# Kernel optimization log

Hardware: AMD Instinct MI355X
Metric: run time of the kernel (lower is better)

The kernel has to match this reference:

```python
import jax, jax.numpy as jnp
import numpy as np

EMBED = 8   # forced: combine_heads Linear(embed_dim, embed_dim) applied to 8-wire measurement
FFN = 32
B, S = 128, 8192
EPS = 1e-5


def _layernorm(x, g, b):
    m = x.mean(-1, keepdims=True)
    v = ((x - m) ** 2).mean(-1, keepdims=True)
    return (x - m) * jax.lax.rsqrt(v + EPS) * g + b


def setup_inputs() -> dict:
    key = jax.random.key(0)
    ks = jax.random.split(key, 8)

    def lin(k, fi, fo):
        return jax.random.normal(k, (fi, fo), jnp.float32) / np.sqrt(fi).astype(np.float32)

    return dict(
        x=jax.random.normal(ks[0], (B, S, EMBED), jnp.float32),
        Wq=lin(ks[1], EMBED, EMBED), bq=jnp.zeros((EMBED,), jnp.float32),
        theta_attn=jax.random.uniform(ks[2], (EMBED,), jnp.float32, -np.pi, np.pi),
        Wc=lin(ks[3], EMBED, EMBED), bc=jnp.zeros((EMBED,), jnp.float32),
        g1=jnp.ones((EMBED,), jnp.float32), beta1=jnp.zeros((EMBED,), jnp.float32),
        theta_ffn=jax.random.uniform(ks[4], (EMBED,), jnp.float32, -np.pi, np.pi),
        W1=lin(ks[5], EMBED, FFN), b1=jnp.zeros((FFN,), jnp.float32),
        W2=lin(ks[6], FFN, EMBED), b2=jnp.zeros((EMBED,), jnp.float32),
        g2=jnp.ones((EMBED,), jnp.float32), beta2=jnp.zeros((EMBED,), jnp.float32),
    )


def reference(x, Wq, bq, theta_attn, Wc, bc, g1, beta1,
              theta_ffn, W1, b1, W2, b2, g2, beta2):
    # --- MultiHeadAttentionQuantum (eval mode, dropout = identity) ---
    # q_linear; the 8-wire encoder consumes all 8 features of q per token.
    q = x @ Wq + bq                           # [B, S, 8]
    # Circuit per token: RX(q_i) then trainable RX(theta_i) on wire i -> RX(q_i+theta_i),
    # then CNOT ring (0->1,...,6->7, 7->0), then <Z_i>.
    # All-RX product state => basis probs p_i(1)=sin^2(a_i/2); CNOTs permute basis
    # states (prefix-XOR of bits), so analytically:
    #   <Z_k> = prod_{j=0..k} cos(a_j)  for k>=1;   <Z_0> = prod_{j=1..7} cos(a_j)
    ca = jnp.cos(q + theta_attn)              # [B, S, 8]
    z_rest = jnp.cumprod(ca, axis=-1)[..., 1:]
    z0 = jnp.prod(ca[..., 1:], axis=-1, keepdims=True)
    z = jnp.concatenate([z0, z_rest], axis=-1)
    attn_out = z @ Wc + bc                    # combine_heads

    x1 = _layernorm(x + attn_out, g1, beta1)

    # --- FeedForwardQuantum: RX(x_i) then RY(theta_i), no entanglers ->
    #     <Z_i> = cos(theta_i) * cos(x_i)  (product state, per-wire closed form)
    zf = jnp.cos(theta_ffn) * jnp.cos(x1)     # [B, S, 8]
    h = jax.nn.relu(zf @ W1 + b1)             # linear1 -> relu
    ffn_out = h @ W2 + b2                     # linear2

    return _layernorm(x1 + ffn_out, g2, beta2)
```

## Files before the change

kernel.cpp:

```cpp
#include <hip/hip_runtime.h>


#define NTOK   (128 * 8192)
#define NTHREADS 256
#define NBLOCKS  (NTOK / NTHREADS)
#define LN_EPS 1e-5f
#define INV2PI 0.15915494309189535f

typedef __fp16 half2_t __attribute__((ext_vector_type(2)));
typedef __fp16 half8_t __attribute__((ext_vector_type(8)));
typedef float  float4_t __attribute__((ext_vector_type(4)));

union PK  { unsigned u; half2_t h; };
union U4H { uint4 u; half8_t h; half2_t h2[4]; };

__device__ __forceinline__ float fast_cos_rev(float xrev) {
    return __builtin_amdgcn_cosf(xrev);
}
__device__ __forceinline__ float fast_cos(float x) {
    return __builtin_amdgcn_cosf(x * INV2PI);
}
__device__ __forceinline__ float fast_rsqrt(float x) {
    return __builtin_amdgcn_rsqf(x);
}
__device__ __forceinline__ unsigned packh2(float a, float b) {
    PK c; c.h = __builtin_amdgcn_cvt_pkrtz(a, b); return c.u;
}
__device__ __forceinline__ float dot2(half2_t a, unsigned bw, float c) {
    PK b; b.u = bw;
    return __builtin_amdgcn_fdot2(a, b.h, c, false);
}

__global__ void pack_weights(const float* __restrict__ Wq,
                             const float* __restrict__ W1,
                             const float* __restrict__ W2,
                             const float* __restrict__ Wc,
                             const float* __restrict__ bq,
                             const float* __restrict__ tha,
                             const float* __restrict__ thf,
                             unsigned* __restrict__ ws)
{
    int idx = threadIdx.x;
    if (idx < 32) {
        int k = idx >> 2, p = idx & 3;
        ws[idx] = packh2(Wq[(2 * p) * 8 + k] * INV2PI, Wq[(2 * p + 1) * 8 + k] * INV2PI);
    } else if (idx < 64) {
        int i2 = idx - 32;
        int kp = i2 >> 3, j = i2 & 7;
        ws[idx] = packh2(Wc[(2 * kp) * 8 + j], Wc[(2 * kp + 1) * 8 + j]);
    } else if (idx < 72) {
        int k = idx - 64;
        ws[idx] = __float_as_uint((bq[k] + tha[k]) * INV2PI);
    } else if (idx < 80) {
        int j = idx - 72;
        ws[idx] = __float_as_uint(__builtin_amdgcn_cosf(thf[j] * INV2PI));
    } else if (idx >= 128 && idx < 320) {
        int t  = (idx - 128) & 63;
        int tb = (idx - 128) >> 6;
        int n0 = t & 15, q = t >> 4;
        uint4 w = make_uint4(0u, 0u, 0u, 0u);
        unsigned r[4] = {0u, 0u, 0u, 0u};
        if (tb == 0) {
            if (q == 0)
                for (int p = 0; p < 4; ++p)
                    r[p] = packh2(W1[(2 * p) * 32 + n0], W1[(2 * p + 1) * 32 + n0]);
        } else if (tb == 1) {
            if (q == 0)
                for (int p = 0; p < 4; ++p)
                    r[p] = packh2(W1[(2 * p) * 32 + n0 + 16], W1[(2 * p + 1) * 32 + n0 + 16]);
        } else {
            if (n0 < 8)
                for (int p = 0; p < 4; ++p)
                    r[p] = packh2(W2[(8 * q + 2 * p) * 8 + n0], W2[(8 * q + 2 * p + 1) * 8 + n0]);
        }
        w.x = r[0]; w.y = r[1]; w.z = r[2]; w.w = r[3];
        reinterpret_cast<uint4*>(ws)[32 + tb * 64 + t] = w;
    }
}

__global__ __launch_bounds__(NTHREADS, 8)
void qtb_kernel(const float* __restrict__ x,
                const float* __restrict__ bc,
                const float* __restrict__ g1,  const float* __restrict__ be1,
                const float* __restrict__ b1,
                const float* __restrict__ b2,
                const float* __restrict__ g2,  const float* __restrict__ be2,
                const unsigned* __restrict__ wp,
                float* __restrict__ out)
{
    const int tid  = threadIdx.x;
    const int wave = tid >> 6;
    const int lane = tid & 63;
    const int col  = lane & 15;
    const int quad = lane >> 4;
    const int g    = blockIdx.x * NTHREADS + tid;

    const float4* px = reinterpret_cast<const float4*>(x) + (size_t)g * 2;
    float4 xa = px[0];
    float4 xb = px[1];

    const float* qb = reinterpret_cast<const float*>(wp + 64);
    const float* cf = reinterpret_cast<const float*>(wp + 72);

    __shared__ uint4    zbuf[4][64];
    __shared__ unsigned hbuf[4][16 * 20];
    __shared__ float    fbuf[4][64 * 9];

    const uint4* fr = reinterpret_cast<const uint4*>(wp);
    U4H B1a, B1b, B2;
    B1a.u = fr[32 + lane];
    B1b.u = fr[96 + lane];
    B2.u  = fr[160 + lane];
    const float b1a_s = b1[col];
    const float b1b_s = b1[col + 16];
    const float b2_s  = (col < 8) ? b2[col & 7] : 0.f;

    float xv[8];
    half2_t xp[4];
    xv[0] = xa.x; xv[1] = xa.y; xv[2] = xa.z; xv[3] = xa.w;
    xv[4] = xb.x; xv[5] = xb.y; xv[6] = xb.z; xv[7] = xb.w;
    xp[0] = __builtin_amdgcn_cvt_pkrtz(xa.x, xa.y);
    xp[1] = __builtin_amdgcn_cvt_pkrtz(xa.z, xa.w);
    xp[2] = __builtin_amdgcn_cvt_pkrtz(xb.x, xb.y);
    xp[3] = __builtin_amdgcn_cvt_pkrtz(xb.z, xb.w);

    float ca[8];
#pragma unroll
    for (int k = 0; k < 8; ++k) {
        float q = qb[k];
#pragma unroll
        for (int p = 0; p < 4; ++p) q = dot2(xp[p], wp[k * 4 + p], q);
        ca[k] = fast_cos_rev(q);
    }
    float attn[8];
#pragma unroll
    for (int j = 0; j < 8; ++j) attn[j] = bc[j];
    {
        float z[8];
        float cp  = ca[0];
        float cp1 = 1.0f;
#pragma unroll
        for (int k = 1; k < 8; ++k) {
            cp  *= ca[k];
            cp1 *= ca[k];
            z[k] = cp;
        }
        z[0] = cp1;
        half2_t zp[4];
#pragma unroll
        for (int p = 0; p < 4; ++p)
            zp[p] = __builtin_amdgcn_cvt_pkrtz(z[2 * p], z[2 * p + 1]);
#pragma unroll
        for (int p = 0; p < 4; ++p)
#pragma unroll
            for (int j = 0; j < 8; ++j)
                attn[j] = dot2(zp[p], wp[32 + p * 8 + j], attn[j]);
    }

    {
        float y[8];
        float s = 0.f;
#pragma unroll
        for (int j = 0; j < 8; ++j) { y[j] = xv[j] + attn[j]; s += y[j]; }
        float m = s * 0.125f;
        float v = 0.f;
#pragma unroll
        for (int j = 0; j < 8; ++j) { float d = y[j] - m; v += d * d; }
        float r = fast_rsqrt(v * 0.125f + LN_EPS);
        float zf[8];
#pragma unroll
        for (int j = 0; j < 8; ++j) {
            float x1 = (y[j] - m) * r * g1[j] + be1[j];
            xv[j] = x1;
            zf[j] = cf[j] * fast_cos(x1);
        }
        U4H zpk;
#pragma unroll
        for (int p = 0; p < 4; ++p)
            zpk.h2[p] = __builtin_amdgcn_cvt_pkrtz(zf[2 * p], zf[2 * p + 1]);
        zbuf[wave][lane] = zpk.u;
    }

    const unsigned psel = (quad < 2) ? 0x05040100u : 0x07060302u;
#pragma unroll
    for (int grp = 0; grp < 4; ++grp) {
        U4H A1; A1.u = zbuf[wave][grp * 16 + col];
        float4_t c1a = {b1a_s, b1a_s, b1a_s, b1a_s};
        float4_t c1b = {b1b_s, b1b_s, b1b_s, b1b_s};
        float4_t h0 = __builtin_amdgcn_mfma_f32_16x16x32_f16(A1.h, B1a.h, c1a, 0, 0, 0);
        float4_t h1 = __builtin_amdgcn_mfma_f32_16x16x32_f16(A1.h, B1b.h, c1b, 0, 0, 0);
#pragma unroll
        for (int r = 0; r < 4; ++r)
            hbuf[wave][(4 * quad + r) * 20 + col] =
                packh2(fmaxf(h0[r], 0.f), fmaxf(h1[r], 0.f));
        int hb = col * 20 + (quad & 1) * 8;
        uint4 w0 = *reinterpret_cast<const uint4*>(&hbuf[wave][hb]);
        uint4 w1 = *reinterpret_cast<const uint4*>(&hbuf[wave][hb + 4]);
        U4H A2;
        A2.u.x = __builtin_amdgcn_perm(w0.y, w0.x, psel);
        A2.u.y = __builtin_amdgcn_perm(w0.w, w0.z, psel);
        A2.u.z = __builtin_amdgcn_perm(w1.y, w1.x, psel);
        A2.u.w = __builtin_amdgcn_perm(w1.w, w1.z, psel);
        float4_t c2 = {b2_s, b2_s, b2_s, b2_s};
        float4_t f = __builtin_amdgcn_mfma_f32_16x16x32_f16(A2.h, B2.h, c2, 0, 0, 0);
        if (col < 8) {
#pragma unroll
            for (int r = 0; r < 4; ++r)
                fbuf[wave][(grp * 16 + 4 * quad + r) * 9 + col] = f[r];
        }
    }

    {
        float y[8];
        float s = 0.f;
#pragma unroll
        for (int j = 0; j < 8; ++j) {
            y[j] = xv[j] + fbuf[wave][lane * 9 + j];
            s += y[j];
        }
        float m = s * 0.125f;
        float v = 0.f;
#pragma unroll
        for (int j = 0; j < 8; ++j) { float d = y[j] - m; v += d * d; }
        float r = fast_rsqrt(v * 0.125f + LN_EPS);
        float o[8];
#pragma unroll
        for (int j = 0; j < 8; ++j) o[j] = (y[j] - m) * r * g2[j] + be2[j];
        float4* q = reinterpret_cast<float4*>(out) + (size_t)g * 2;
        q[0] = make_float4(o[0], o[1], o[2], o[3]);
        q[1] = make_float4(o[4], o[5], o[6], o[7]);
    }
}

extern "C" void kernel_launch(void* const* d_in, const int* in_sizes, int n_in,
                              void* d_out, int out_size, void* d_ws, size_t ws_size,
                              hipStream_t stream) {
    (void)in_sizes; (void)n_in; (void)ws_size; (void)out_size;
    unsigned* wp = (unsigned*)d_ws;
    pack_weights<<<1, 320, 0, stream>>>(
        (const float*)d_in[1],
        (const float*)d_in[9],
        (const float*)d_in[11],
        (const float*)d_in[4],
        (const float*)d_in[2],
        (const float*)d_in[3],
        (const float*)d_in[8],
        wp);
    qtb_kernel<<<NBLOCKS, NTHREADS, 0, stream>>>(
        (const float*)d_in[0],
        (const float*)d_in[5],
        (const float*)d_in[6],
        (const float*)d_in[7],
        (const float*)d_in[10],
        (const float*)d_in[12],
        (const float*)d_in[13],
        (const float*)d_in[14],
        wp,
        (float*)d_out);
}
```

Before: 115.0 us.

## Replace MFMA FFN with per-thread packed fp16 dot2 FFN

Drops the matrix-core path for the feed-forward layers, along with its LDS staging buffers and shuffles. Each thread now evaluates both FFN linears for its own token with packed fp16 dot2 instructions, reading the packed weights as uniform scalar loads from the workspace. This removes shared-memory traffic and cross-lane data movement. In exchange it raises per-thread VALU work (32x4 plus 8x16 dot2 ops) and register pressure.

```diff
diff --git a/kernel.cpp b/kernel.cpp
--- a/kernel.cpp
+++ b/kernel.cpp
@@ -8,11 +8,8 @@
 #define INV2PI 0.15915494309189535f
 
 typedef __fp16 half2_t __attribute__((ext_vector_type(2)));
-typedef __fp16 half8_t __attribute__((ext_vector_type(8)));
-typedef float  float4_t __attribute__((ext_vector_type(4)));
 
 union PK  { unsigned u; half2_t h; };
-union U4H { uint4 u; half8_t h; half2_t h2[4]; };
 
 __device__ __forceinline__ float fast_cos_rev(float xrev) {
     return __builtin_amdgcn_cosf(xrev);
@@ -54,27 +51,14 @@
     } else if (idx < 80) {
         int j = idx - 72;
         ws[idx] = __float_as_uint(__builtin_amdgcn_cosf(thf[j] * INV2PI));
-    } else if (idx >= 128 && idx < 320) {
-        int t  = (idx - 128) & 63;
-        int tb = (idx - 128) >> 6;
-        int n0 = t & 15, q = t >> 4;
-        uint4 w = make_uint4(0u, 0u, 0u, 0u);
-        unsigned r[4] = {0u, 0u, 0u, 0u};
-        if (tb == 0) {
-            if (q == 0)
-                for (int p = 0; p < 4; ++p)
-                    r[p] = packh2(W1[(2 * p) * 32 + n0], W1[(2 * p + 1) * 32 + n0]);
-        } else if (tb == 1) {
-            if (q == 0)
-                for (int p = 0; p < 4; ++p)
-                    r[p] = packh2(W1[(2 * p) * 32 + n0 + 16], W1[(2 * p + 1) * 32 + n0 + 16]);
-        } else {
-            if (n0 < 8)
-                for (int p = 0; p < 4; ++p)
-                    r[p] = packh2(W2[(8 * q + 2 * p) * 8 + n0], W2[(8 * q + 2 * p + 1) * 8 + n0]);
-        }
-        w.x = r[0]; w.y = r[1]; w.z = r[2]; w.w = r[3];
-        reinterpret_cast<uint4*>(ws)[32 + tb * 64 + t] = w;
+    } else if (idx < 208) {
+        int i = idx - 80;
+        int p = i >> 5, n = i & 31;
+        ws[idx] = packh2(W1[(2 * p) * 32 + n], W1[(2 * p + 1) * 32 + n]);
+    } else if (idx < 336) {
+        int i = idx - 208;
+        int p = i >> 3, j = i & 7;
+        ws[idx] = packh2(W2[(2 * p) * 8 + j], W2[(2 * p + 1) * 8 + j]);
     }
 }
 
@@ -88,12 +72,7 @@
                 const unsigned* __restrict__ wp,
                 float* __restrict__ out)
 {
-    const int tid  = threadIdx.x;
-    const int wave = tid >> 6;
-    const int lane = tid & 63;
-    const int col  = lane & 15;
-    const int quad = lane >> 4;
-    const int g    = blockIdx.x * NTHREADS + tid;
+    const int g = blockIdx.x * NTHREADS + threadIdx.x;
 
     const float4* px = reinterpret_cast<const float4*>(x) + (size_t)g * 2;
     float4 xa = px[0];
@@ -101,19 +80,6 @@
 
     const float* qb = reinterpret_cast<const float*>(wp + 64);
     const float* cf = reinterpret_cast<const float*>(wp + 72);
-
-    __shared__ uint4    zbuf[4][64];
-    __shared__ unsigned hbuf[4][16 * 20];
-    __shared__ float    fbuf[4][64 * 9];
-
-    const uint4* fr = reinterpret_cast<const uint4*>(wp);
-    U4H B1a, B1b, B2;
-    B1a.u = fr[32 + lane];
-    B1b.u = fr[96 + lane];
-    B2.u  = fr[160 + lane];
-    const float b1a_s = b1[col];
-    const float b1b_s = b1[col + 16];
-    const float b2_s  = (col < 8) ? b2[col & 7] : 0.f;
 
     float xv[8];
     half2_t xp[4];
@@ -157,6 +123,7 @@
                 attn[j] = dot2(zp[p], wp[32 + p * 8 + j], attn[j]);
     }
 
+    half2_t zp2[4];
     {
         float y[8];
         float s = 0.f;
@@ -174,61 +141,52 @@
             xv[j] = x1;
             zf[j] = cf[j] * fast_cos(x1);
         }
-        U4H zpk;
-#pragma unroll
-        for (int p = 0; p < 4; ++p)
-            zpk.h2[p] = __builtin_amdgcn_cvt_pkrtz(zf[2 * p], zf[2 * p + 1]);
-        zbuf[wave][lane] = zpk.u;
-    }
-
-    const unsigned psel = (quad < 2) ? 0x05040100u : 0x07060302u;
-#pragma unroll
-    for (int grp = 0; grp < 4; ++grp) {
-        U4H A1; A1.u = zbuf[wave][grp * 16 + col];
-        float4_t c1a = {b1a_s, b1a_s, b1a_s, b1a_s};
-        float4_t c1b = {b1b_s, b1b_s, b1b_s, b1b_s};
-        float4_t h0 = __builtin_amdgcn_mfma_f32_16x16x32_f16(A1.h, B1a.h, c1a, 0, 0, 0);
-        float4_t h1 = __builtin_amdgcn_mfma_f32_16x16x32_f16(A1.h, B1b.h, c1b, 0, 0, 0);
-#pragma unroll
-        for (int r = 0; r < 4; ++r)
-            hbuf[wave][(4 * quad + r) * 20 + col] =
-                packh2(fmaxf(h0[r], 0.f), fmaxf(h1[r], 0.f));
-        int hb = col * 20 + (quad & 1) * 8;
-        uint4 w0 = *reinterpret_cast<const uint4*>(&hbuf[wave][hb]);
-        uint4 w1 = *reinterpret_cast<const uint4*>(&hbuf[wave][hb + 4]);
-        U4H A2;
-        A2.u.x = __builtin_amdgcn_perm(w0.y, w0.x, psel);
-        A2.u.y = __builtin_amdgcn_perm(w0.w, w0.z, psel);
-        A2.u.z = __builtin_amdgcn_perm(w1.y, w1.x, psel);
-        A2.u.w = __builtin_amdgcn_perm(w1.w, w1.z, psel);
-        float4_t c2 = {b2_s, b2_s, b2_s, b2_s};
-        float4_t f = __builtin_amdgcn_mfma_f32_16x16x32_f16(A2.h, B2.h, c2, 0, 0, 0);
-        if (col < 8) {
-#pragma unroll
-            for (int r = 0; r < 4; ++r)
-                fbuf[wave][(grp * 16 + 4 * quad + r) * 9 + col] = f[r];
-        }
-    }
+#pragma unroll
+        for (int p = 0; p < 4; ++p)
+            zp2[p] = __builtin_amdgcn_cvt_pkrtz(zf[2 * p], zf[2 * p + 1]);
+    }
+
+    half2_t hp[16];
+#pragma unroll
+    for (int c = 0; c < 2; ++c) {
+        float acc[16];
+#pragma unroll
+        for (int n = 0; n < 16; ++n) acc[n] = b1[c * 16 + n];
+#pragma unroll
+        for (int p = 0; p < 4; ++p)
+#pragma unroll
+            for (int n = 0; n < 16; ++n)
+                acc[n] = dot2(zp2[p], wp[80 + p * 32 + c * 16 + n], acc[n]);
+#pragma unroll
+        for (int n2 = 0; n2 < 8; ++n2)
+            hp[c * 8 + n2] = __builtin_amdgcn_cvt_pkrtz(fmaxf(acc[2 * n2], 0.f),
+                                                        fmaxf(acc[2 * n2 + 1], 0.f));
+    }
+    float o[8];
+#pragma unroll
+    for (int j = 0; j < 8; ++j) o[j] = b2[j];
+#pragma unroll
+    for (int p = 0; p < 16; ++p)
+#pragma unroll
+        for (int j = 0; j < 8; ++j)
+            o[j] = dot2(hp[p], wp[208 + p * 8 + j], o[j]);
 
     {
         float y[8];
         float s = 0.f;
 #pragma unroll
-        for (int j = 0; j < 8; ++j) {
-            y[j] = xv[j] + fbuf[wave][lane * 9 + j];
-            s += y[j];
-        }
+        for (int j = 0; j < 8; ++j) { y[j] = xv[j] + o[j]; s += y[j]; }
         float m = s * 0.125f;
         float v = 0.f;
 #pragma unroll
         for (int j = 0; j < 8; ++j) { float d = y[j] - m; v += d * d; }
         float r = fast_rsqrt(v * 0.125f + LN_EPS);
-        float o[8];
-#pragma unroll
-        for (int j = 0; j < 8; ++j) o[j] = (y[j] - m) * r * g2[j] + be2[j];
+        float ov[8];
+#pragma unroll
+        for (int j = 0; j < 8; ++j) ov[j] = (y[j] - m) * r * g2[j] + be2[j];
         float4* q = reinterpret_cast<float4*>(out) + (size_t)g * 2;
-        q[0] = make_float4(o[0], o[1], o[2], o[3]);
-        q[1] = make_float4(o[4], o[5], o[6], o[7]);
+        q[0] = make_float4(ov[0], ov[1], ov[2], ov[3]);
+        q[1] = make_float4(ov[4], ov[5], ov[6], ov[7]);
     }
 }
 
@@ -237,7 +195,7 @@
                               hipStream_t stream) {
     (void)in_sizes; (void)n_in; (void)ws_size; (void)out_size;
     unsigned* wp = (unsigned*)d_ws;
-    pack_weights<<<1, 320, 0, stream>>>(
+    pack_weights<<<1, 384, 0, stream>>>(
         (const float*)d_in[1],
         (const float*)d_in[9],
         (const float*)d_in[11],
```

Result: slower. 118.6 us (+3.1%).
